# Performance work log

Hardware: AMD Instinct MI355X
Metric: run time of the kernel (lower is better)

Reference implementation:

```python
import jax, jax.numpy as jnp
import numpy as np

NUM_BINS_X = 512
NUM_BINS_Y = 512
XL, YL, XH, YH = 0.0, 0.0, 1.0, 1.0
ROUTING_H = 50000.0
ROUTING_V = 50000.0
MACRO_UTIL_H = 10.0
MACRO_UTIL_V = 10.0
NUM_NETS = 131072
PINS_PER_NET = 4
NUM_MOVABLE = 50000
NUM_TERMINALS = 5000
NUM_NODES = NUM_MOVABLE + NUM_TERMINALS
NUM_PINS = NUM_NETS * PINS_PER_NET
BIN_SIZE_X = (XH - XL) / NUM_BINS_X
BIN_SIZE_Y = (YH - YL) / NUM_BINS_Y


def setup_inputs():
    key = jax.random.key(0)
    k1, k2, k3, k4 = jax.random.split(key, 4)
    # pin_pos = [x_0..x_P-1, y_0..y_P-1], pos = [x_0..x_N-1, y_0..y_N-1]
    pin_pos = jax.random.uniform(k1, (2 * NUM_PINS,), dtype=jnp.float32, minval=XL, maxval=XH)
    pos = jax.random.uniform(k2, (2 * NUM_NODES,), dtype=jnp.float32, minval=XL, maxval=0.9 * (XH - XL))
    node_size_x = jax.random.uniform(k3, (NUM_NODES,), dtype=jnp.float32, minval=0.01, maxval=0.05)
    node_size_y = jax.random.uniform(k4, (NUM_NODES,), dtype=jnp.float32, minval=0.01, maxval=0.05)
    net_weights = jnp.ones((NUM_NETS,), jnp.float32)
    rng = np.random.default_rng(0)
    flat_netpin = jnp.asarray(rng.permutation(NUM_PINS).astype(np.int32))
    movable = rng.choice(NUM_MOVABLE, 64, replace=False)
    fixed = NUM_MOVABLE + rng.choice(NUM_TERMINALS, 32, replace=False)
    macro_indexes = jnp.asarray(np.concatenate([movable, fixed]).astype(np.int32))
    return dict(pos=pos, pin_pos=pin_pos, node_size_x=node_size_x, node_size_y=node_size_y,
                net_weights=net_weights, flat_netpin=flat_netpin, macro_indexes=macro_indexes)


def _bin_overlap(lo, hi, origin, bin_size, num_bins):
    # [N, num_bins]: overlap length of interval [lo, hi] with each bin along one axis
    edges = origin + bin_size * jnp.arange(num_bins, dtype=lo.dtype)
    return jnp.clip(jnp.minimum(hi[:, None], edges[None, :] + bin_size)
                    - jnp.maximum(lo[:, None], edges[None, :]), 0.0, None)


def _blur3(m, sigma):
    # torchvision GaussianBlur(kernel_size=3, sigma), separable, reflect padding
    x = jnp.array([-1.0, 0.0, 1.0], m.dtype)
    k = jnp.exp(-0.5 * (x / sigma) ** 2)
    k = k / k.sum()
    mp = jnp.pad(m, ((1, 1), (0, 0)), mode='reflect')
    m = k[0] * mp[:-2] + k[1] * mp[1:-1] + k[2] * mp[2:]
    mp = jnp.pad(m, ((0, 0), (1, 1)), mode='reflect')
    return k[0] * mp[:, :-2] + k[1] * mp[:, 1:-1] + k[2] * mp[:, 2:]


def _rudy_maps(pos, pin_pos, node_size_x, node_size_y, net_weights, flat_netpin, macro_indexes):
    # net bounding boxes from pins (fixed PINS_PER_NET pins per net)
    px = pin_pos[:NUM_PINS][flat_netpin].reshape(NUM_NETS, PINS_PER_NET)
    py = pin_pos[NUM_PINS:][flat_netpin].reshape(NUM_NETS, PINS_PER_NET)
    x_min, x_max = px.min(1), px.max(1)
    y_min, y_max = py.min(1), py.max(1)
    ox = _bin_overlap(x_min, x_max, XL, BIN_SIZE_X, NUM_BINS_X)   # [N, Bx]
    oy = _bin_overlap(y_min, y_max, YL, BIN_SIZE_Y, NUM_BINS_Y)   # [N, By]
    wh = net_weights / (y_max - y_min)  # RUDY horizontal demand density
    wv = net_weights / (x_max - x_min)  # RUDY vertical demand density
    H = jnp.einsum('nx,ny->xy', ox * wh[:, None], oy)
    V = jnp.einsum('nx,ny->xy', ox * wv[:, None], oy)
    # macro contributions
    mx = pos[macro_indexes]
    my = pos[NUM_NODES + macro_indexes]
    msx = node_size_x[macro_indexes]
    msy = node_size_y[macro_indexes]
    area = msx * msy
    mox = _bin_overlap(mx, mx + msx, XL, BIN_SIZE_X, NUM_BINS_X)
    moy = _bin_overlap(my, my + msy, YL, BIN_SIZE_Y, NUM_BINS_Y)
    H = H + jnp.einsum('mx,my->xy', mox * (MACRO_UTIL_H / area)[:, None], moy)
    V = V + jnp.einsum('mx,my->xy', mox * (MACRO_UTIL_V / area)[:, None], moy)
    num_bins = NUM_BINS_X * NUM_BINS_Y
    H = H / (ROUTING_H / num_bins)
    V = V / (ROUTING_V / num_bins)
    sigma = min((XH - XL) / BIN_SIZE_X, (YH - YL) / BIN_SIZE_Y) / 16.0
    return _blur3(H, sigma), _blur3(V, sigma)


def reference(pos, pin_pos, node_size_x, node_size_y, net_weights, flat_netpin, macro_indexes):
    H, V = _rudy_maps(pos, pin_pos, node_size_x, node_size_y, net_weights, flat_netpin, macro_indexes)
    h_ov = jnp.maximum(H - 1.0, 0.0)
    v_ov = jnp.maximum(V - 1.0, 0.0)
    h_cnt = (h_ov > 0).sum()
    v_cnt = (v_ov > 0).sum()
    total_overflow = h_cnt + v_cnt          # total overflow bin area
    max_overflow = jnp.maximum(h_cnt, v_cnt)  # jit-compatible proxy for largest contour area
    route_utilization_map = jnp.maximum(jnp.abs(H), jnp.abs(V))
    return route_utilization_map, max_overflow, total_overflow
```

## Files before the change

### kernel.cpp

```cpp
#include <hip/hip_runtime.h>

#define N_NETS  131072
#define N_PINS  (N_NETS * 4)
#define N_NODES 55000
#define NRECMAX (N_NETS + 128)
#define NBBLK   129
#define NPARTS  4
#define CELLCAP 160

struct __align__(16) Meta { uint2 cols; float2 whv; float4 pys; };

__device__ uint4 g_pair[NRECMAX * 2];
__device__ Meta  g_meta[NRECMAX];
__device__ unsigned short g_cellcnt[64 * NBBLK];
__device__ unsigned g_cell[64 * NBBLK * CELLCAP];
__device__ float g_part[NPARTS * 512 * 1024];
__device__ int   g_cnt2[2];
__device__ int   g_tick;

__global__ __launch_bounds__(1024) void k_bbox(
    const float* __restrict__ pos, const float* __restrict__ pin_pos,
    const float* __restrict__ nsx, const float* __restrict__ nsy,
    const float* __restrict__ nw,  const int* __restrict__ fnp,
    const int* __restrict__ mid, int nm)
{
    __shared__ unsigned s_stage[64 * CELLCAP];
    __shared__ int s_cnt[64];
    int tid = threadIdx.x;
    int b = blockIdx.x;
    int t = b * 1024 + tid;
    if (b == 0 && tid == 0) { g_cnt2[0] = 0; g_cnt2[1] = 0; g_tick = 0; }
    if (tid < 64) s_cnt[tid] = 0;
    __syncthreads();

    auto append = [&](int s, unsigned ent) {
        int off = atomicAdd(&s_cnt[s], 1);
        if (off < CELLCAP) s_stage[s * CELLCAP + off] = ent;
    };

    bool valid = t < N_NETS + nm && t < NRECMAX;
    if (valid) {
        float xmin, xmax, ymin, ymax, wh, wv;
        if (t < N_NETS) {
            int4 p = ((const int4*)fnp)[t];
            float x0 = pin_pos[p.x], x1 = pin_pos[p.y], x2 = pin_pos[p.z], x3 = pin_pos[p.w];
            float y0 = pin_pos[N_PINS + p.x], y1 = pin_pos[N_PINS + p.y];
            float y2 = pin_pos[N_PINS + p.z], y3 = pin_pos[N_PINS + p.w];
            xmin = fminf(fminf(x0, x1), fminf(x2, x3));
            xmax = fmaxf(fmaxf(x0, x1), fmaxf(x2, x3));
            ymin = fminf(fminf(y0, y1), fminf(y2, y3));
            ymax = fmaxf(fmaxf(y0, y1), fmaxf(y2, y3));
            float w = nw[t];
            wh = w / (ymax - ymin);
            wv = w / (xmax - xmin);
        } else {
            int idx = mid[t - N_NETS];
            xmin = pos[idx]; ymin = pos[N_NODES + idx];
            float sx = nsx[idx], sy = nsy[idx];
            xmax = xmin + sx; ymax = ymin + sy;
            wh = wv = 10.0f / (sx * sy);
        }
        const float B = 1.0f / 512.0f;
        int xl = min(max((int)(xmin * 512.0f), 0), 511);
        int xh = min(max((int)(xmax * 512.0f), 0), 511);
        int yl = min(max((int)(ymin * 512.0f), 0), 511);
        int yh = min(max((int)(ymax * 512.0f), 0), 511);
        g_pair[2 * t] = make_uint4(
            (unsigned)xl | ((unsigned)(xl + 1) << 16),
            __float_as_uint((xl + 1) * B - xmin),
            __float_as_uint(xmin - xl * B), 0u);
        g_pair[2 * t + 1] = make_uint4(
            (unsigned)xh | ((unsigned)(xh + 1) << 16),
            __float_as_uint(xmax - (xh + 1) * B),
            __float_as_uint(xh * B - xmax), 0u);
        Meta m;
        m.cols = make_uint2((unsigned)yl | ((unsigned)(yl + 1) << 16),
                            (unsigned)yh | ((unsigned)(yh + 1) << 16));
        m.whv = make_float2(wh, wv);
        m.pys = make_float4((yl + 1) * B - ymin, ymin - yl * B,
                            ymax - (yh + 1) * B, yh * B - ymax);
        g_meta[t] = m;
        append(xl & 63,        ((unsigned)t << 2) | 0u);
        if (xl + 1 < 512) append((xl + 1) & 63, ((unsigned)t << 2) | 1u);
        append(xh & 63,        ((unsigned)t << 2) | 2u);
        if (xh + 1 < 512) append((xh + 1) & 63, ((unsigned)t << 2) | 3u);
    }
    __syncthreads();
    if (tid < 64) g_cellcnt[tid * NBBLK + b] = (unsigned short)min(s_cnt[tid], CELLCAP);
    int wid = tid >> 6, lane = tid & 63;
    for (int s = wid; s < 64; s += 16) {
        int n = min(s_cnt[s], CELLCAP);
        unsigned* dst = &g_cell[(unsigned)(s * NBBLK + b) * CELLCAP];
        for (int k = lane; k < n; k += 64) dst[k] = s_stage[s * CELLCAP + k];
    }
}

__global__ __launch_bounds__(1024) void k_deposit() {
    __shared__ float tile[8706];
    __shared__ int s_pref[64];
    __shared__ int s_total;
    int tid = threadIdx.x;
    int s = blockIdx.x >> 2, p = blockIdx.x & 3;
#pragma unroll
    for (int k = tid; k < 8706; k += 1024) tile[k] = 0.0f;

    int lob = (NBBLK * p) >> 2, hib = (NBBLK * (p + 1)) >> 2;
    int nb = hib - lob;
    if (tid < 64) {
        int c = (tid < nb) ? (int)g_cellcnt[s * NBBLK + lob + tid] : 0;
        int v = c;
#pragma unroll
        for (int off = 1; off < 64; off <<= 1) {
            int tv = __shfl_up(v, off);
            if (tid >= off) v += tv;
        }
        s_pref[tid] = v - c;
        if (tid == 63) s_total = v;
    }
    __syncthreads();

    int total = s_total;
    for (int k = tid; k < total; k += 1024) {
        int loJ = 0, hiJ = 63;
#pragma unroll
        for (int st = 0; st < 6; ++st) {
            int mid = (loJ + hiJ + 1) >> 1;
            if (s_pref[mid] <= k) loJ = mid; else hiJ = mid - 1;
        }
        int bb = lob + loJ;
        int idx = k - s_pref[loJ];
        unsigned ent = g_cell[(unsigned)(s * NBBLK + bb) * CELLCAP + idx];
        int i = (int)(ent >> 2);
        int e = (int)(ent & 3u);
        uint4 pw = g_pair[2 * i + (e >> 1)];
        int row = (e & 1) ? (int)(pw.x >> 16) : (int)(pw.x & 0xFFFFu);
        float px = __uint_as_float((e & 1) ? pw.z : pw.y);
        Meta m = g_meta[i];
        float ah = px * m.whv.x, av = px * m.whv.y;
        int base = (row >> 6) * 1024;
        unsigned c0 = m.cols.x & 0xFFFFu, c1 = m.cols.x >> 16;
        unsigned c2 = m.cols.y & 0xFFFFu, c3 = m.cols.y >> 16;
        int i0 = (c0 < 512u) ? base + 2 * (int)c0 : 8192;
        int i1 = (c1 < 512u) ? base + 2 * (int)c1 : 8192;
        int i2 = (c2 < 512u) ? base + 2 * (int)c2 : 8192;
        int i3 = (c3 < 512u) ? base + 2 * (int)c3 : 8192;
        unsafeAtomicAdd(&tile[i0],     ah * m.pys.x);
        unsafeAtomicAdd(&tile[i0 + 1], av * m.pys.x);
        unsafeAtomicAdd(&tile[i1],     ah * m.pys.y);
        unsafeAtomicAdd(&tile[i1 + 1], av * m.pys.y);
        unsafeAtomicAdd(&tile[i2],     ah * m.pys.z);
        unsafeAtomicAdd(&tile[i2 + 1], av * m.pys.z);
        unsafeAtomicAdd(&tile[i3],     ah * m.pys.w);
        unsafeAtomicAdd(&tile[i3 + 1], av * m.pys.w);
    }
    __syncthreads();

    int wid = tid >> 6, lane = tid & 63;
    if (wid < 8) {
        float2* rowp = (float2*)&tile[wid * 1024];
        float cx = 0.0f, cy = 0.0f;
        for (int ch = 0; ch < 8; ++ch) {
            float2 v = rowp[ch * 64 + lane];
#pragma unroll
            for (int off = 1; off < 64; off <<= 1) {
                float tx = __shfl_up(v.x, off);
                float ty = __shfl_up(v.y, off);
                if (lane >= off) { v.x += tx; v.y += ty; }
            }
            v.x += cx; v.y += cy;
            rowp[ch * 64 + lane] = v;
            cx = __shfl(v.x, 63); cy = __shfl(v.y, 63);
        }
    }
    __syncthreads();
    int dstp = p * 524288 + (s << 10);
#pragma unroll
    for (int k = 0; k < 8; ++k) {
        int idx = tid + k * 1024;
        int rr = idx >> 10, cc = idx & 1023;
        g_part[dstp + (rr << 16) + cc] = tile[idx];
    }
}

__global__ __launch_bounds__(1024) void k_finish(float* __restrict__ out) {
    __shared__ float sB[16 * 512];
    int tid = threadIdx.x;
    int b = blockIdx.x;
    int lane = tid & 63;
    int c20 = tid & 31;
    int xg = tid >> 5;
    int jj = (c20 < 10) ? c20 : c20 - 10;
    int cy = 8 * b - 1 + jj;
    if (cy < 0) cy = 1;
    if (cy > 511) cy = 510;
    int map = (c20 < 10) ? 0 : 1;
    int gcol = 2 * cy + map;
    const float kw  = expf(-0.5f / 1024.0f);
    const float k1n = 1.0f / (1.0f + 2.0f * kw);
    const float k0n = kw * k1n;
    const float scale = 262144.0f / 50000.0f;
    bool active = c20 < 20;
    int t8  = (c20 < 10) ? c20 - 1 : c20 - 11;

    for (int xo = 0; xo < 16; ++xo) {
        int x = xo * 32 + xg;
        float v = 0.0f;
        if (active) {
            int base = x * 1024 + gcol;
#pragma unroll
            for (int p = 0; p < NPARTS; ++p) v += g_part[p * 524288 + base];
        }
        float vm = __shfl(v, lane - 1);
        float vp = __shfl(v, lane + 1);
        float yb = (k0n * (vm + vp) + k1n * v) * scale;
        if (t8 >= 0 && t8 < 8) sB[(map * 8 + t8) * 512 + x] = yb;
    }
    __syncthreads();

    int w = tid >> 6;
    float s0,s1,s2,s3,s4,s5,s6,s7;
    {
        float4 a  = *(float4*)&sB[w * 512 + lane * 8];
        float4 bq = *(float4*)&sB[w * 512 + lane * 8 + 4];
        s0 = a.x; s1 = s0 + a.y; s2 = s1 + a.z; s3 = s2 + a.w;
        s4 = s3 + bq.x; s5 = s4 + bq.y; s6 = s5 + bq.z; s7 = s6 + bq.w;
        float tot = s7;
#pragma unroll
        for (int off = 1; off < 64; off <<= 1) {
            float tv = __shfl_up(tot, off);
            if (lane >= off) tot += tv;
        }
        float e = tot - s7;
        s0 += e; s1 += e; s2 += e; s3 += e; s4 += e; s5 += e; s6 += e; s7 += e;
    }
    {
        float prev = __shfl(s7, lane - 1);
        float next = __shfl(s0, lane + 1);
        float pm = (lane == 0) ? s1 : prev;
        float nx = (lane == 63) ? s6 : next;
        float b0 = k0n * (pm + s1) + k1n * s0;
        float b1 = k0n * (s0 + s2) + k1n * s1;
        float b2 = k0n * (s1 + s3) + k1n * s2;
        float b3 = k0n * (s2 + s4) + k1n * s3;
        float b4 = k0n * (s3 + s5) + k1n * s4;
        float b5 = k0n * (s4 + s6) + k1n * s5;
        float b6 = k0n * (s5 + s7) + k1n * s6;
        float b7 = k0n * (s6 + nx) + k1n * s7;
        float* row = &sB[w * 512 + lane * 8];
        row[0]=b0; row[1]=b1; row[2]=b2; row[3]=b3;
        row[4]=b4; row[5]=b5; row[6]=b6; row[7]=b7;
    }
    __syncthreads();

    int x = tid >> 1, qh = (tid & 1) * 4;
    float4 o;
    int ch = 0, cv = 0;
#pragma unroll
    for (int k = 0; k < 4; ++k) {
        int tt = qh + k;
        float hv = sB[tt * 512 + x];
        float vv = sB[(8 + tt) * 512 + x];
        ((float*)&o)[k] = fmaxf(fabsf(hv), fabsf(vv));
        ch += (hv > 1.0f); cv += (vv > 1.0f);
    }
    *(float4*)&out[x * 512 + 8 * b + qh] = o;
#pragma unroll
    for (int off = 32; off > 0; off >>= 1) {
        ch += __shfl_down(ch, off);
        cv += __shfl_down(cv, off);
    }
    __shared__ int scnt[2];
    if (tid < 2) scnt[tid] = 0;
    __syncthreads();
    if (lane == 0) { atomicAdd(&scnt[0], ch); atomicAdd(&scnt[1], cv); }
    __syncthreads();
    if (tid == 0) {
        atomicAdd(&g_cnt2[0], scnt[0]);
        atomicAdd(&g_cnt2[1], scnt[1]);
        __threadfence();
        int old = atomicAdd(&g_tick, 1);
        if (old == 63) {
            __threadfence();
            int h = g_cnt2[0], v = g_cnt2[1];
            out[262144] = (float)((h > v) ? h : v);
            out[262145] = (float)(h + v);
        }
    }
}

extern "C" void kernel_launch(void* const* d_in, const int* in_sizes, int n_in,
                              void* d_out, int out_size, void* d_ws, size_t ws_size,
                              hipStream_t stream) {
    const float* pos     = (const float*)d_in[0];
    const float* pin_pos = (const float*)d_in[1];
    const float* nsx     = (const float*)d_in[2];
    const float* nsy     = (const float*)d_in[3];
    const float* nw      = (const float*)d_in[4];
    const int*   fnp     = (const int*)d_in[5];
    const int*   mid     = (const int*)d_in[6];
    int nm = in_sizes[6];
    float* out = (float*)d_out;

    hipLaunchKernelGGL(k_bbox,    dim3(NBBLK), dim3(1024), 0, stream,
                       pos, pin_pos, nsx, nsy, nw, fnp, mid, nm);
    hipLaunchKernelGGL(k_deposit, dim3(256), dim3(1024), 0, stream);
    hipLaunchKernelGGL(k_finish,  dim3(64), dim3(1024), 0, stream, out);
}
```

Baseline: 63.62 us.

## Fuse three kernels into one cooperative persistent kernel with grid barriers

Merges the bbox, deposit and finish stages into a single cooperative launch of 256 blocks, separated by software grid barriers built on monotonic atomic counters. The bbox stage now spreads records over 256 blocks of 513 nets, so the x-cell buckets line up one-to-one with the deposit partitions, and the per-cell capacity shrinks to fit. This removes two kernel launch gaps and the drain between stages. The cost is barrier spin overhead, only one block per CU, and a risk of silently dropping entries if a bucket overflows the smaller capacity.

Measured after the change: 231.9 us. +264.4%, slower.

```diff
diff --git a/kernel.cpp b/kernel.cpp
--- a/kernel.cpp
+++ b/kernel.cpp
@@ -3,287 +3,317 @@
 #define N_NETS  131072
 #define N_PINS  (N_NETS * 4)
 #define N_NODES 55000
-#define NRECMAX (N_NETS + 128)
-#define NBBLK   129
+#define NBLK    256
+#define RPB     513
 #define NPARTS  4
-#define CELLCAP 160
+#define CELLCAP 112
 
 struct __align__(16) Meta { uint2 cols; float2 whv; float4 pys; };
 
-__device__ uint4 g_pair[NRECMAX * 2];
-__device__ Meta  g_meta[NRECMAX];
-__device__ unsigned short g_cellcnt[64 * NBBLK];
-__device__ unsigned g_cell[64 * NBBLK * CELLCAP];
+__device__ uint4 g_pair[(N_NETS + 128) * 2];
+__device__ Meta  g_meta[N_NETS + 128];
+__device__ unsigned short g_cellcnt[64 * NBLK];
+__device__ unsigned g_cell[64 * NBLK * CELLCAP];
 __device__ float g_part[NPARTS * 512 * 1024];
-__device__ int   g_cnt2[2];
-__device__ int   g_tick;
-
-__global__ __launch_bounds__(1024) void k_bbox(
+__device__ int      g_cnt2[2];
+__device__ unsigned g_tick;
+__device__ unsigned g_bar1, g_bar2;
+
+__device__ __forceinline__ void bar_wait(unsigned* bar, int tid) {
+    __syncthreads();
+    __threadfence();
+    if (tid == 0) {
+        unsigned old = atomicAdd(bar, 1u);
+        unsigned tgt = (old & ~255u) + 256u;
+        while (__hip_atomic_load(bar, __ATOMIC_ACQUIRE, __HIP_MEMORY_SCOPE_AGENT) < tgt)
+            __builtin_amdgcn_s_sleep(8);
+        __threadfence();
+    }
+    __syncthreads();
+}
+
+__global__ __launch_bounds__(1024) void k_all(
     const float* __restrict__ pos, const float* __restrict__ pin_pos,
     const float* __restrict__ nsx, const float* __restrict__ nsy,
     const float* __restrict__ nw,  const int* __restrict__ fnp,
-    const int* __restrict__ mid, int nm)
+    const int* __restrict__ mid, int nm, float* __restrict__ out)
 {
-    __shared__ unsigned s_stage[64 * CELLCAP];
-    __shared__ int s_cnt[64];
+    __shared__ __align__(16) unsigned char s_raw[35840];
+    __shared__ int s_pref[64];
+    __shared__ int s_total;
+    __shared__ int scnt[2];
     int tid = threadIdx.x;
     int b = blockIdx.x;
-    int t = b * 1024 + tid;
-    if (b == 0 && tid == 0) { g_cnt2[0] = 0; g_cnt2[1] = 0; g_tick = 0; }
-    if (tid < 64) s_cnt[tid] = 0;
+
+    {
+        unsigned* s_stage = (unsigned*)s_raw;
+        int* s_cnt = (int*)(s_raw + 64 * CELLCAP * 4);
+        if (tid < 64) s_cnt[tid] = 0;
+        __syncthreads();
+
+        auto append = [&](int s, unsigned ent) {
+            int off = atomicAdd(&s_cnt[s], 1);
+            if (off < CELLCAP) s_stage[s * CELLCAP + off] = ent;
+        };
+
+        int t = b * RPB + tid;
+        if (tid < RPB && t < N_NETS + nm) {
+            float xmin, xmax, ymin, ymax, wh, wv;
+            if (t < N_NETS) {
+                int4 p = ((const int4*)fnp)[t];
+                float x0 = pin_pos[p.x], x1 = pin_pos[p.y], x2 = pin_pos[p.z], x3 = pin_pos[p.w];
+                float y0 = pin_pos[N_PINS + p.x], y1 = pin_pos[N_PINS + p.y];
+                float y2 = pin_pos[N_PINS + p.z], y3 = pin_pos[N_PINS + p.w];
+                xmin = fminf(fminf(x0, x1), fminf(x2, x3));
+                xmax = fmaxf(fmaxf(x0, x1), fmaxf(x2, x3));
+                ymin = fminf(fminf(y0, y1), fminf(y2, y3));
+                ymax = fmaxf(fmaxf(y0, y1), fmaxf(y2, y3));
+                float w = nw[t];
+                wh = w / (ymax - ymin);
+                wv = w / (xmax - xmin);
+            } else {
+                int idx = mid[t - N_NETS];
+                xmin = pos[idx]; ymin = pos[N_NODES + idx];
+                float sx = nsx[idx], sy = nsy[idx];
+                xmax = xmin + sx; ymax = ymin + sy;
+                wh = wv = 10.0f / (sx * sy);
+            }
+            const float B = 1.0f / 512.0f;
+            int xl = min(max((int)(xmin * 512.0f), 0), 511);
+            int xh = min(max((int)(xmax * 512.0f), 0), 511);
+            int yl = min(max((int)(ymin * 512.0f), 0), 511);
+            int yh = min(max((int)(ymax * 512.0f), 0), 511);
+            g_pair[2 * t] = make_uint4(
+                (unsigned)xl | ((unsigned)(xl + 1) << 16),
+                __float_as_uint((xl + 1) * B - xmin),
+                __float_as_uint(xmin - xl * B), 0u);
+            g_pair[2 * t + 1] = make_uint4(
+                (unsigned)xh | ((unsigned)(xh + 1) << 16),
+                __float_as_uint(xmax - (xh + 1) * B),
+                __float_as_uint(xh * B - xmax), 0u);
+            Meta m;
+            m.cols = make_uint2((unsigned)yl | ((unsigned)(yl + 1) << 16),
+                                (unsigned)yh | ((unsigned)(yh + 1) << 16));
+            m.whv = make_float2(wh, wv);
+            m.pys = make_float4((yl + 1) * B - ymin, ymin - yl * B,
+                                ymax - (yh + 1) * B, yh * B - ymax);
+            g_meta[t] = m;
+            append(xl & 63,        ((unsigned)t << 2) | 0u);
+            if (xl + 1 < 512) append((xl + 1) & 63, ((unsigned)t << 2) | 1u);
+            append(xh & 63,        ((unsigned)t << 2) | 2u);
+            if (xh + 1 < 512) append((xh + 1) & 63, ((unsigned)t << 2) | 3u);
+        }
+        __syncthreads();
+        if (tid < 64) g_cellcnt[tid * NBLK + b] = (unsigned short)min(s_cnt[tid], CELLCAP);
+        int wid = tid >> 6, lane = tid & 63;
+        for (int s = wid; s < 64; s += 16) {
+            int n = min(s_cnt[s], CELLCAP);
+            unsigned* dst = &g_cell[(unsigned)(s * NBLK + b) * CELLCAP];
+            for (int k = lane; k < n; k += 64) dst[k] = s_stage[s * CELLCAP + k];
+        }
+    }
+    bar_wait(&g_bar1, tid);
+
+    {
+        float* tile = (float*)s_raw;
+        int s = b >> 2, p = b & 3;
+#pragma unroll
+        for (int k = tid; k < 8706; k += 1024) tile[k] = 0.0f;
+
+        int cb0 = p * 64;
+        if (tid < 64) {
+            int c = (int)g_cellcnt[s * NBLK + cb0 + tid];
+            int v = c;
+#pragma unroll
+            for (int off = 1; off < 64; off <<= 1) {
+                int tv = __shfl_up(v, off);
+                if (tid >= off) v += tv;
+            }
+            s_pref[tid] = v - c;
+            if (tid == 63) s_total = v;
+        }
+        __syncthreads();
+
+        int total = s_total;
+        for (int k = tid; k < total; k += 1024) {
+            int loJ = 0, hiJ = 63;
+#pragma unroll
+            for (int st = 0; st < 6; ++st) {
+                int mid_ = (loJ + hiJ + 1) >> 1;
+                if (s_pref[mid_] <= k) loJ = mid_; else hiJ = mid_ - 1;
+            }
+            int idx = k - s_pref[loJ];
+            unsigned ent = g_cell[(unsigned)(s * NBLK + cb0 + loJ) * CELLCAP + idx];
+            int i = (int)(ent >> 2);
+            int e = (int)(ent & 3u);
+            uint4 pw = g_pair[2 * i + (e >> 1)];
+            int row = (e & 1) ? (int)(pw.x >> 16) : (int)(pw.x & 0xFFFFu);
+            float px = __uint_as_float((e & 1) ? pw.z : pw.y);
+            Meta m = g_meta[i];
+            float ah = px * m.whv.x, av = px * m.whv.y;
+            int base = (row >> 6) * 1024;
+            unsigned c0 = m.cols.x & 0xFFFFu, c1 = m.cols.x >> 16;
+            unsigned c2 = m.cols.y & 0xFFFFu, c3 = m.cols.y >> 16;
+            int i0 = (c0 < 512u) ? base + 2 * (int)c0 : 8192;
+            int i1 = (c1 < 512u) ? base + 2 * (int)c1 : 8192;
+            int i2 = (c2 < 512u) ? base + 2 * (int)c2 : 8192;
+            int i3 = (c3 < 512u) ? base + 2 * (int)c3 : 8192;
+            unsafeAtomicAdd(&tile[i0],     ah * m.pys.x);
+            unsafeAtomicAdd(&tile[i0 + 1], av * m.pys.x);
+            unsafeAtomicAdd(&tile[i1],     ah * m.pys.y);
+            unsafeAtomicAdd(&tile[i1 + 1], av * m.pys.y);
+            unsafeAtomicAdd(&tile[i2],     ah * m.pys.z);
+            unsafeAtomicAdd(&tile[i2 + 1], av * m.pys.z);
+            unsafeAtomicAdd(&tile[i3],     ah * m.pys.w);
+            unsafeAtomicAdd(&tile[i3 + 1], av * m.pys.w);
+        }
+        __syncthreads();
+
+        int wid = tid >> 6, lane = tid & 63;
+        if (wid < 8) {
+            float2* rowp = (float2*)&tile[wid * 1024];
+            float cx = 0.0f, cy = 0.0f;
+            for (int ch = 0; ch < 8; ++ch) {
+                float2 v = rowp[ch * 64 + lane];
+#pragma unroll
+                for (int off = 1; off < 64; off <<= 1) {
+                    float tx = __shfl_up(v.x, off);
+                    float ty = __shfl_up(v.y, off);
+                    if (lane >= off) { v.x += tx; v.y += ty; }
+                }
+                v.x += cx; v.y += cy;
+                rowp[ch * 64 + lane] = v;
+                cx = __shfl(v.x, 63); cy = __shfl(v.y, 63);
+            }
+        }
+        __syncthreads();
+        int dstp = p * 524288 + (s << 10);
+#pragma unroll
+        for (int k = 0; k < 8; ++k) {
+            int idx = tid + k * 1024;
+            int rr = idx >> 10, cc = idx & 1023;
+            g_part[dstp + (rr << 16) + cc] = tile[idx];
+        }
+    }
+
     __syncthreads();
-
-    auto append = [&](int s, unsigned ent) {
-        int off = atomicAdd(&s_cnt[s], 1);
-        if (off < CELLCAP) s_stage[s * CELLCAP + off] = ent;
-    };
-
-    bool valid = t < N_NETS + nm && t < NRECMAX;
-    if (valid) {
-        float xmin, xmax, ymin, ymax, wh, wv;
-        if (t < N_NETS) {
-            int4 p = ((const int4*)fnp)[t];
-            float x0 = pin_pos[p.x], x1 = pin_pos[p.y], x2 = pin_pos[p.z], x3 = pin_pos[p.w];
-            float y0 = pin_pos[N_PINS + p.x], y1 = pin_pos[N_PINS + p.y];
-            float y2 = pin_pos[N_PINS + p.z], y3 = pin_pos[N_PINS + p.w];
-            xmin = fminf(fminf(x0, x1), fminf(x2, x3));
-            xmax = fmaxf(fmaxf(x0, x1), fmaxf(x2, x3));
-            ymin = fminf(fminf(y0, y1), fminf(y2, y3));
-            ymax = fmaxf(fmaxf(y0, y1), fmaxf(y2, y3));
-            float w = nw[t];
-            wh = w / (ymax - ymin);
-            wv = w / (xmax - xmin);
-        } else {
-            int idx = mid[t - N_NETS];
-            xmin = pos[idx]; ymin = pos[N_NODES + idx];
-            float sx = nsx[idx], sy = nsy[idx];
-            xmax = xmin + sx; ymax = ymin + sy;
-            wh = wv = 10.0f / (sx * sy);
-        }
-        const float B = 1.0f / 512.0f;
-        int xl = min(max((int)(xmin * 512.0f), 0), 511);
-        int xh = min(max((int)(xmax * 512.0f), 0), 511);
-        int yl = min(max((int)(ymin * 512.0f), 0), 511);
-        int yh = min(max((int)(ymax * 512.0f), 0), 511);
-        g_pair[2 * t] = make_uint4(
-            (unsigned)xl | ((unsigned)(xl + 1) << 16),
-            __float_as_uint((xl + 1) * B - xmin),
-            __float_as_uint(xmin - xl * B), 0u);
-        g_pair[2 * t + 1] = make_uint4(
-            (unsigned)xh | ((unsigned)(xh + 1) << 16),
-            __float_as_uint(xmax - (xh + 1) * B),
-            __float_as_uint(xh * B - xmax), 0u);
-        Meta m;
-        m.cols = make_uint2((unsigned)yl | ((unsigned)(yl + 1) << 16),
-                            (unsigned)yh | ((unsigned)(yh + 1) << 16));
-        m.whv = make_float2(wh, wv);
-        m.pys = make_float4((yl + 1) * B - ymin, ymin - yl * B,
-                            ymax - (yh + 1) * B, yh * B - ymax);
-        g_meta[t] = m;
-        append(xl & 63,        ((unsigned)t << 2) | 0u);
-        if (xl + 1 < 512) append((xl + 1) & 63, ((unsigned)t << 2) | 1u);
-        append(xh & 63,        ((unsigned)t << 2) | 2u);
-        if (xh + 1 < 512) append((xh + 1) & 63, ((unsigned)t << 2) | 3u);
+    __threadfence();
+    if (b >= 64) {
+        if (tid == 0) atomicAdd(&g_bar2, 1u);
+        return;
+    }
+    if (tid == 0) {
+        unsigned old = atomicAdd(&g_bar2, 1u);
+        unsigned tgt = (old & ~255u) + 256u;
+        while (__hip_atomic_load(&g_bar2, __ATOMIC_ACQUIRE, __HIP_MEMORY_SCOPE_AGENT) < tgt)
+            __builtin_amdgcn_s_sleep(8);
+        __threadfence();
     }
     __syncthreads();
-    if (tid < 64) g_cellcnt[tid * NBBLK + b] = (unsigned short)min(s_cnt[tid], CELLCAP);
-    int wid = tid >> 6, lane = tid & 63;
-    for (int s = wid; s < 64; s += 16) {
-        int n = min(s_cnt[s], CELLCAP);
-        unsigned* dst = &g_cell[(unsigned)(s * NBBLK + b) * CELLCAP];
-        for (int k = lane; k < n; k += 64) dst[k] = s_stage[s * CELLCAP + k];
-    }
-}
-
-__global__ __launch_bounds__(1024) void k_deposit() {
-    __shared__ float tile[8706];
-    __shared__ int s_pref[64];
-    __shared__ int s_total;
-    int tid = threadIdx.x;
-    int s = blockIdx.x >> 2, p = blockIdx.x & 3;
-#pragma unroll
-    for (int k = tid; k < 8706; k += 1024) tile[k] = 0.0f;
-
-    int lob = (NBBLK * p) >> 2, hib = (NBBLK * (p + 1)) >> 2;
-    int nb = hib - lob;
-    if (tid < 64) {
-        int c = (tid < nb) ? (int)g_cellcnt[s * NBBLK + lob + tid] : 0;
-        int v = c;
-#pragma unroll
-        for (int off = 1; off < 64; off <<= 1) {
-            int tv = __shfl_up(v, off);
-            if (tid >= off) v += tv;
-        }
-        s_pref[tid] = v - c;
-        if (tid == 63) s_total = v;
-    }
-    __syncthreads();
-
-    int total = s_total;
-    for (int k = tid; k < total; k += 1024) {
-        int loJ = 0, hiJ = 63;
-#pragma unroll
-        for (int st = 0; st < 6; ++st) {
-            int mid = (loJ + hiJ + 1) >> 1;
-            if (s_pref[mid] <= k) loJ = mid; else hiJ = mid - 1;
-        }
-        int bb = lob + loJ;
-        int idx = k - s_pref[loJ];
-        unsigned ent = g_cell[(unsigned)(s * NBBLK + bb) * CELLCAP + idx];
-        int i = (int)(ent >> 2);
-        int e = (int)(ent & 3u);
-        uint4 pw = g_pair[2 * i + (e >> 1)];
-        int row = (e & 1) ? (int)(pw.x >> 16) : (int)(pw.x & 0xFFFFu);
-        float px = __uint_as_float((e & 1) ? pw.z : pw.y);
-        Meta m = g_meta[i];
-        float ah = px * m.whv.x, av = px * m.whv.y;
-        int base = (row >> 6) * 1024;
-        unsigned c0 = m.cols.x & 0xFFFFu, c1 = m.cols.x >> 16;
-        unsigned c2 = m.cols.y & 0xFFFFu, c3 = m.cols.y >> 16;
-        int i0 = (c0 < 512u) ? base + 2 * (int)c0 : 8192;
-        int i1 = (c1 < 512u) ? base + 2 * (int)c1 : 8192;
-        int i2 = (c2 < 512u) ? base + 2 * (int)c2 : 8192;
-        int i3 = (c3 < 512u) ? base + 2 * (int)c3 : 8192;
-        unsafeAtomicAdd(&tile[i0],     ah * m.pys.x);
-        unsafeAtomicAdd(&tile[i0 + 1], av * m.pys.x);
-        unsafeAtomicAdd(&tile[i1],     ah * m.pys.y);
-        unsafeAtomicAdd(&tile[i1 + 1], av * m.pys.y);
-        unsafeAtomicAdd(&tile[i2],     ah * m.pys.z);
-        unsafeAtomicAdd(&tile[i2 + 1], av * m.pys.z);
-        unsafeAtomicAdd(&tile[i3],     ah * m.pys.w);
-        unsafeAtomicAdd(&tile[i3 + 1], av * m.pys.w);
-    }
-    __syncthreads();
-
-    int wid = tid >> 6, lane = tid & 63;
-    if (wid < 8) {
-        float2* rowp = (float2*)&tile[wid * 1024];
-        float cx = 0.0f, cy = 0.0f;
-        for (int ch = 0; ch < 8; ++ch) {
-            float2 v = rowp[ch * 64 + lane];
+
+    {
+        float* sB = (float*)s_raw;
+        int lane = tid & 63;
+        int c20 = tid & 31;
+        int xg = tid >> 5;
+        int jj = (c20 < 10) ? c20 : c20 - 10;
+        int cy = 8 * b - 1 + jj;
+        if (cy < 0) cy = 1;
+        if (cy > 511) cy = 510;
+        int map = (c20 < 10) ? 0 : 1;
+        int gcol = 2 * cy + map;
+        const float kw  = expf(-0.5f / 1024.0f);
+        const float k1n = 1.0f / (1.0f + 2.0f * kw);
+        const float k0n = kw * k1n;
+        const float scale = 262144.0f / 50000.0f;
+        bool active = c20 < 20;
+        int t8  = (c20 < 10) ? c20 - 1 : c20 - 11;
+
+        for (int xo = 0; xo < 16; ++xo) {
+            int x = xo * 32 + xg;
+            float v = 0.0f;
+            if (active) {
+                int base = x * 1024 + gcol;
+#pragma unroll
+                for (int p = 0; p < NPARTS; ++p) v += g_part[p * 524288 + base];
+            }
+            float vm = __shfl(v, lane - 1);
+            float vp = __shfl(v, lane + 1);
+            float yb = (k0n * (vm + vp) + k1n * v) * scale;
+            if (t8 >= 0 && t8 < 8) sB[(map * 8 + t8) * 512 + x] = yb;
+        }
+        __syncthreads();
+
+        int w = tid >> 6;
+        float s0,s1,s2,s3,s4,s5,s6,s7;
+        {
+            float4 a  = *(float4*)&sB[w * 512 + lane * 8];
+            float4 bq = *(float4*)&sB[w * 512 + lane * 8 + 4];
+            s0 = a.x; s1 = s0 + a.y; s2 = s1 + a.z; s3 = s2 + a.w;
+            s4 = s3 + bq.x; s5 = s4 + bq.y; s6 = s5 + bq.z; s7 = s6 + bq.w;
+            float tot = s7;
 #pragma unroll
             for (int off = 1; off < 64; off <<= 1) {
-                float tx = __shfl_up(v.x, off);
-                float ty = __shfl_up(v.y, off);
-                if (lane >= off) { v.x += tx; v.y += ty; }
-            }
-            v.x += cx; v.y += cy;
-            rowp[ch * 64 + lane] = v;
-            cx = __shfl(v.x, 63); cy = __shfl(v.y, 63);
-        }
-    }
-    __syncthreads();
-    int dstp = p * 524288 + (s << 10);
-#pragma unroll
-    for (int k = 0; k < 8; ++k) {
-        int idx = tid + k * 1024;
-        int rr = idx >> 10, cc = idx & 1023;
-        g_part[dstp + (rr << 16) + cc] = tile[idx];
-    }
-}
-
-__global__ __launch_bounds__(1024) void k_finish(float* __restrict__ out) {
-    __shared__ float sB[16 * 512];
-    int tid = threadIdx.x;
-    int b = blockIdx.x;
-    int lane = tid & 63;
-    int c20 = tid & 31;
-    int xg = tid >> 5;
-    int jj = (c20 < 10) ? c20 : c20 - 10;
-    int cy = 8 * b - 1 + jj;
-    if (cy < 0) cy = 1;
-    if (cy > 511) cy = 510;
-    int map = (c20 < 10) ? 0 : 1;
-    int gcol = 2 * cy + map;
-    const float kw  = expf(-0.5f / 1024.0f);
-    const float k1n = 1.0f / (1.0f + 2.0f * kw);
-    const float k0n = kw * k1n;
-    const float scale = 262144.0f / 50000.0f;
-    bool active = c20 < 20;
-    int t8  = (c20 < 10) ? c20 - 1 : c20 - 11;
-
-    for (int xo = 0; xo < 16; ++xo) {
-        int x = xo * 32 + xg;
-        float v = 0.0f;
-        if (active) {
-            int base = x * 1024 + gcol;
-#pragma unroll
-            for (int p = 0; p < NPARTS; ++p) v += g_part[p * 524288 + base];
-        }
-        float vm = __shfl(v, lane - 1);
-        float vp = __shfl(v, lane + 1);
-        float yb = (k0n * (vm + vp) + k1n * v) * scale;
-        if (t8 >= 0 && t8 < 8) sB[(map * 8 + t8) * 512 + x] = yb;
-    }
-    __syncthreads();
-
-    int w = tid >> 6;
-    float s0,s1,s2,s3,s4,s5,s6,s7;
-    {
-        float4 a  = *(float4*)&sB[w * 512 + lane * 8];
-        float4 bq = *(float4*)&sB[w * 512 + lane * 8 + 4];
-        s0 = a.x; s1 = s0 + a.y; s2 = s1 + a.z; s3 = s2 + a.w;
-        s4 = s3 + bq.x; s5 = s4 + bq.y; s6 = s5 + bq.z; s7 = s6 + bq.w;
-        float tot = s7;
-#pragma unroll
-        for (int off = 1; off < 64; off <<= 1) {
-            float tv = __shfl_up(tot, off);
-            if (lane >= off) tot += tv;
-        }
-        float e = tot - s7;
-        s0 += e; s1 += e; s2 += e; s3 += e; s4 += e; s5 += e; s6 += e; s7 += e;
-    }
-    {
-        float prev = __shfl(s7, lane - 1);
-        float next = __shfl(s0, lane + 1);
-        float pm = (lane == 0) ? s1 : prev;
-        float nx = (lane == 63) ? s6 : next;
-        float b0 = k0n * (pm + s1) + k1n * s0;
-        float b1 = k0n * (s0 + s2) + k1n * s1;
-        float b2 = k0n * (s1 + s3) + k1n * s2;
-        float b3 = k0n * (s2 + s4) + k1n * s3;
-        float b4 = k0n * (s3 + s5) + k1n * s4;
-        float b5 = k0n * (s4 + s6) + k1n * s5;
-        float b6 = k0n * (s5 + s7) + k1n * s6;
-        float b7 = k0n * (s6 + nx) + k1n * s7;
-        float* row = &sB[w * 512 + lane * 8];
-        row[0]=b0; row[1]=b1; row[2]=b2; row[3]=b3;
-        row[4]=b4; row[5]=b5; row[6]=b6; row[7]=b7;
-    }
-    __syncthreads();
-
-    int x = tid >> 1, qh = (tid & 1) * 4;
-    float4 o;
-    int ch = 0, cv = 0;
-#pragma unroll
-    for (int k = 0; k < 4; ++k) {
-        int tt = qh + k;
-        float hv = sB[tt * 512 + x];
-        float vv = sB[(8 + tt) * 512 + x];
-        ((float*)&o)[k] = fmaxf(fabsf(hv), fabsf(vv));
-        ch += (hv > 1.0f); cv += (vv > 1.0f);
-    }
-    *(float4*)&out[x * 512 + 8 * b + qh] = o;
-#pragma unroll
-    for (int off = 32; off > 0; off >>= 1) {
-        ch += __shfl_down(ch, off);
-        cv += __shfl_down(cv, off);
-    }
-    __shared__ int scnt[2];
-    if (tid < 2) scnt[tid] = 0;
-    __syncthreads();
-    if (lane == 0) { atomicAdd(&scnt[0], ch); atomicAdd(&scnt[1], cv); }
-    __syncthreads();
-    if (tid == 0) {
-        atomicAdd(&g_cnt2[0], scnt[0]);
-        atomicAdd(&g_cnt2[1], scnt[1]);
-        __threadfence();
-        int old = atomicAdd(&g_tick, 1);
-        if (old == 63) {
+                float tv = __shfl_up(tot, off);
+                if (lane >= off) tot += tv;
+            }
+            float e = tot - s7;
+            s0 += e; s1 += e; s2 += e; s3 += e; s4 += e; s5 += e; s6 += e; s7 += e;
+        }
+        {
+            float prev = __shfl(s7, lane - 1);
+            float next = __shfl(s0, lane + 1);
+            float pm = (lane == 0) ? s1 : prev;
+            float nx = (lane == 63) ? s6 : next;
+            float b0 = k0n * (pm + s1) + k1n * s0;
+            float b1 = k0n * (s0 + s2) + k1n * s1;
+            float b2 = k0n * (s1 + s3) + k1n * s2;
+            float b3 = k0n * (s2 + s4) + k1n * s3;
+            float b4 = k0n * (s3 + s5) + k1n * s4;
+            float b5 = k0n * (s4 + s6) + k1n * s5;
+            float b6 = k0n * (s5 + s7) + k1n * s6;
+            float b7 = k0n * (s6 + nx) + k1n * s7;
+            float* row = &sB[w * 512 + lane * 8];
+            row[0]=b0; row[1]=b1; row[2]=b2; row[3]=b3;
+            row[4]=b4; row[5]=b5; row[6]=b6; row[7]=b7;
+        }
+        __syncthreads();
+
+        int x = tid >> 1, qh = (tid & 1) * 4;
+        float4 o;
+        int ch = 0, cv = 0;
+#pragma unroll
+        for (int k = 0; k < 4; ++k) {
+            int tt = qh + k;
+            float hv = sB[tt * 512 + x];
+            float vv = sB[(8 + tt) * 512 + x];
+            ((float*)&o)[k] = fmaxf(fabsf(hv), fabsf(vv));
+            ch += (hv > 1.0f); cv += (vv > 1.0f);
+        }
+        *(float4*)&out[x * 512 + 8 * b + qh] = o;
+#pragma unroll
+        for (int off = 32; off > 0; off >>= 1) {
+            ch += __shfl_down(ch, off);
+            cv += __shfl_down(cv, off);
+        }
+        if (tid < 2) scnt[tid] = 0;
+        __syncthreads();
+        if (lane == 0) { atomicAdd(&scnt[0], ch); atomicAdd(&scnt[1], cv); }
+        __syncthreads();
+        if (tid == 0) {
+            atomicAdd(&g_cnt2[0], scnt[0]);
+            atomicAdd(&g_cnt2[1], scnt[1]);
             __threadfence();
-            int h = g_cnt2[0], v = g_cnt2[1];
-            out[262144] = (float)((h > v) ? h : v);
-            out[262145] = (float)(h + v);
+            unsigned old = atomicAdd(&g_tick, 1u);
+            if ((old & 63u) == 63u) {
+                __threadfence();
+                int h = atomicAdd(&g_cnt2[0], 0);
+                int v = atomicAdd(&g_cnt2[1], 0);
+                out[262144] = (float)((h > v) ? h : v);
+                out[262145] = (float)(h + v);
+                atomicExch(&g_cnt2[0], 0);
+                atomicExch(&g_cnt2[1], 0);
+            }
         }
     }
 }
@@ -300,9 +330,8 @@
     const int*   mid     = (const int*)d_in[6];
     int nm = in_sizes[6];
     float* out = (float*)d_out;
-
-    hipLaunchKernelGGL(k_bbox,    dim3(NBBLK), dim3(1024), 0, stream,
-                       pos, pin_pos, nsx, nsy, nw, fnp, mid, nm);
-    hipLaunchKernelGGL(k_deposit, dim3(256), dim3(1024), 0, stream);
-    hipLaunchKernelGGL(k_finish,  dim3(64), dim3(1024), 0, stream, out);
+    void* args[] = { (void*)&pos, (void*)&pin_pos, (void*)&nsx, (void*)&nsy,
+                     (void*)&nw, (void*)&fnp, (void*)&mid, (void*)&nm, (void*)&out };
+    hipLaunchCooperativeKernel((const void*)k_all, dim3(NBLK), dim3(1024),
+                               args, 0, stream);
 }
```

## Write self-contained deposit entries directly to bucketed global storage

Applied to the files above, without the earlier changes.

The bbox kernel now writes a fully self-contained 32-byte entry (column indices, row group, pre-multiplied weights, y-overlaps) straight into per-cell global slots. This replaces the shared-memory staging, the indirect net index, and the separate pair/meta arrays. The deposit kernel then reads two contiguous uint4 values per entry instead of chasing an index and gathering scattered records, which removes a dependent random global load. In exchange, more bytes are written per entry with scattered stores, and the cell capacity drops from 160 to 128, which raises overflow risk. The final reduction's tick logic is also changed to use modulo and atomic reads.

New measurement: 66.35 us. 1.04x slower.

```diff
diff --git a/kernel.cpp b/kernel.cpp
--- a/kernel.cpp
+++ b/kernel.cpp
@@ -3,20 +3,15 @@
 #define N_NETS  131072
 #define N_PINS  (N_NETS * 4)
 #define N_NODES 55000
-#define NRECMAX (N_NETS + 128)
 #define NBBLK   129
 #define NPARTS  4
-#define CELLCAP 160
-
-struct __align__(16) Meta { uint2 cols; float2 whv; float4 pys; };
-
-__device__ uint4 g_pair[NRECMAX * 2];
-__device__ Meta  g_meta[NRECMAX];
+#define CELLCAP 128
+
+__device__ uint4 g_ent[64 * NBBLK * CELLCAP * 2];
 __device__ unsigned short g_cellcnt[64 * NBBLK];
-__device__ unsigned g_cell[64 * NBBLK * CELLCAP];
 __device__ float g_part[NPARTS * 512 * 1024];
-__device__ int   g_cnt2[2];
-__device__ int   g_tick;
+__device__ int      g_cnt2[2];
+__device__ unsigned g_tick;
 
 __global__ __launch_bounds__(1024) void k_bbox(
     const float* __restrict__ pos, const float* __restrict__ pin_pos,
@@ -24,7 +19,6 @@
     const float* __restrict__ nw,  const int* __restrict__ fnp,
     const int* __restrict__ mid, int nm)
 {
-    __shared__ unsigned s_stage[64 * CELLCAP];
     __shared__ int s_cnt[64];
     int tid = threadIdx.x;
     int b = blockIdx.x;
@@ -33,13 +27,7 @@
     if (tid < 64) s_cnt[tid] = 0;
     __syncthreads();
 
-    auto append = [&](int s, unsigned ent) {
-        int off = atomicAdd(&s_cnt[s], 1);
-        if (off < CELLCAP) s_stage[s * CELLCAP + off] = ent;
-    };
-
-    bool valid = t < N_NETS + nm && t < NRECMAX;
-    if (valid) {
+    if (t < N_NETS + nm) {
         float xmin, xmax, ymin, ymax, wh, wv;
         if (t < N_NETS) {
             int4 p = ((const int4*)fnp)[t];
@@ -65,34 +53,34 @@
         int xh = min(max((int)(xmax * 512.0f), 0), 511);
         int yl = min(max((int)(ymin * 512.0f), 0), 511);
         int yh = min(max((int)(ymax * 512.0f), 0), 511);
-        g_pair[2 * t] = make_uint4(
-            (unsigned)xl | ((unsigned)(xl + 1) << 16),
-            __float_as_uint((xl + 1) * B - xmin),
-            __float_as_uint(xmin - xl * B), 0u);
-        g_pair[2 * t + 1] = make_uint4(
-            (unsigned)xh | ((unsigned)(xh + 1) << 16),
-            __float_as_uint(xmax - (xh + 1) * B),
-            __float_as_uint(xh * B - xmax), 0u);
-        Meta m;
-        m.cols = make_uint2((unsigned)yl | ((unsigned)(yl + 1) << 16),
-                            (unsigned)yh | ((unsigned)(yh + 1) << 16));
-        m.whv = make_float2(wh, wv);
-        m.pys = make_float4((yl + 1) * B - ymin, ymin - yl * B,
-                            ymax - (yh + 1) * B, yh * B - ymax);
-        g_meta[t] = m;
-        append(xl & 63,        ((unsigned)t << 2) | 0u);
-        if (xl + 1 < 512) append((xl + 1) & 63, ((unsigned)t << 2) | 1u);
-        append(xh & 63,        ((unsigned)t << 2) | 2u);
-        if (xh + 1 < 512) append((xh + 1) & 63, ((unsigned)t << 2) | 3u);
+        unsigned w0c = (unsigned)yl | ((unsigned)(yl + 1) << 16);
+        unsigned w1c = (unsigned)yh | ((unsigned)(yh + 1) << 16);
+        float4 pys = make_float4((yl + 1) * B - ymin, ymin - yl * B,
+                                 ymax - (yh + 1) * B, yh * B - ymax);
+        uint4 Bq = make_uint4(__float_as_uint(pys.x), __float_as_uint(pys.y),
+                              __float_as_uint(pys.z), __float_as_uint(pys.w));
+
+        auto put = [&](int row, float px) {
+            int s = row & 63;
+            int slot = atomicAdd(&s_cnt[s], 1);
+            if (slot < CELLCAP) {
+                uint4 A;
+                A.x = w0c | ((unsigned)(row >> 6) << 29);
+                A.y = w1c;
+                A.z = __float_as_uint(px * wh);
+                A.w = __float_as_uint(px * wv);
+                unsigned base = ((unsigned)(s * NBBLK + b) * CELLCAP + (unsigned)slot) * 2u;
+                g_ent[base]     = A;
+                g_ent[base + 1] = Bq;
+            }
+        };
+        put(xl, (xl + 1) * B - xmin);
+        if (xl + 1 < 512) put(xl + 1, xmin - xl * B);
+        put(xh, xmax - (xh + 1) * B);
+        if (xh + 1 < 512) put(xh + 1, xh * B - xmax);
     }
     __syncthreads();
     if (tid < 64) g_cellcnt[tid * NBBLK + b] = (unsigned short)min(s_cnt[tid], CELLCAP);
-    int wid = tid >> 6, lane = tid & 63;
-    for (int s = wid; s < 64; s += 16) {
-        int n = min(s_cnt[s], CELLCAP);
-        unsigned* dst = &g_cell[(unsigned)(s * NBBLK + b) * CELLCAP];
-        for (int k = lane; k < n; k += 64) dst[k] = s_stage[s * CELLCAP + k];
-    }
 }
 
 __global__ __launch_bounds__(1024) void k_deposit() {
@@ -124,34 +112,32 @@
         int loJ = 0, hiJ = 63;
 #pragma unroll
         for (int st = 0; st < 6; ++st) {
-            int mid = (loJ + hiJ + 1) >> 1;
-            if (s_pref[mid] <= k) loJ = mid; else hiJ = mid - 1;
-        }
-        int bb = lob + loJ;
-        int idx = k - s_pref[loJ];
-        unsigned ent = g_cell[(unsigned)(s * NBBLK + bb) * CELLCAP + idx];
-        int i = (int)(ent >> 2);
-        int e = (int)(ent & 3u);
-        uint4 pw = g_pair[2 * i + (e >> 1)];
-        int row = (e & 1) ? (int)(pw.x >> 16) : (int)(pw.x & 0xFFFFu);
-        float px = __uint_as_float((e & 1) ? pw.z : pw.y);
-        Meta m = g_meta[i];
-        float ah = px * m.whv.x, av = px * m.whv.y;
-        int base = (row >> 6) * 1024;
-        unsigned c0 = m.cols.x & 0xFFFFu, c1 = m.cols.x >> 16;
-        unsigned c2 = m.cols.y & 0xFFFFu, c3 = m.cols.y >> 16;
+            int mid_ = (loJ + hiJ + 1) >> 1;
+            if (s_pref[mid_] <= k) loJ = mid_; else hiJ = mid_ - 1;
+        }
+        unsigned gidx = ((unsigned)(s * NBBLK + lob + loJ) * CELLCAP
+                         + (unsigned)(k - s_pref[loJ])) * 2u;
+        uint4 A  = g_ent[gidx];
+        uint4 Bq = g_ent[gidx + 1];
+        int rr = (int)(A.x >> 29);
+        unsigned c0 = A.x & 0xFFFFu, c1 = (A.x >> 16) & 0x1FFFu;
+        unsigned c2 = A.y & 0xFFFFu, c3 = A.y >> 16;
+        float ah = __uint_as_float(A.z), av = __uint_as_float(A.w);
+        float p0 = __uint_as_float(Bq.x), p1 = __uint_as_float(Bq.y);
+        float p2 = __uint_as_float(Bq.z), p3 = __uint_as_float(Bq.w);
+        int base = rr * 1024;
         int i0 = (c0 < 512u) ? base + 2 * (int)c0 : 8192;
         int i1 = (c1 < 512u) ? base + 2 * (int)c1 : 8192;
         int i2 = (c2 < 512u) ? base + 2 * (int)c2 : 8192;
         int i3 = (c3 < 512u) ? base + 2 * (int)c3 : 8192;
-        unsafeAtomicAdd(&tile[i0],     ah * m.pys.x);
-        unsafeAtomicAdd(&tile[i0 + 1], av * m.pys.x);
-        unsafeAtomicAdd(&tile[i1],     ah * m.pys.y);
-        unsafeAtomicAdd(&tile[i1 + 1], av * m.pys.y);
-        unsafeAtomicAdd(&tile[i2],     ah * m.pys.z);
-        unsafeAtomicAdd(&tile[i2 + 1], av * m.pys.z);
-        unsafeAtomicAdd(&tile[i3],     ah * m.pys.w);
-        unsafeAtomicAdd(&tile[i3 + 1], av * m.pys.w);
+        unsafeAtomicAdd(&tile[i0],     ah * p0);
+        unsafeAtomicAdd(&tile[i0 + 1], av * p0);
+        unsafeAtomicAdd(&tile[i1],     ah * p1);
+        unsafeAtomicAdd(&tile[i1 + 1], av * p1);
+        unsafeAtomicAdd(&tile[i2],     ah * p2);
+        unsafeAtomicAdd(&tile[i2 + 1], av * p2);
+        unsafeAtomicAdd(&tile[i3],     ah * p3);
+        unsafeAtomicAdd(&tile[i3 + 1], av * p3);
     }
     __syncthreads();
 
@@ -278,10 +264,11 @@
         atomicAdd(&g_cnt2[0], scnt[0]);
         atomicAdd(&g_cnt2[1], scnt[1]);
         __threadfence();
-        int old = atomicAdd(&g_tick, 1);
-        if (old == 63) {
+        unsigned old = atomicAdd(&g_tick, 1u);
+        if ((old & 63u) == 63u) {
             __threadfence();
-            int h = g_cnt2[0], v = g_cnt2[1];
+            int h = atomicAdd(&g_cnt2[0], 0);
+            int v = atomicAdd(&g_cnt2[1], 0);
             out[262144] = (float)((h > v) ? h : v);
             out[262145] = (float)(h + v);
         }
```
